# Kernel tuning notes

Measured on AMD Instinct MI355X. Metric: run time of the kernel, lower is better.

The kernel has to match this reference:

```python
import jax, jax.numpy as jnp
import numpy as np

B, L, W = 4096, 30, 5          # batch, MAX_TOKEN_LENGTH, WINDOW_SIZE
A, E = 30, 128                 # ALPHABET_SIZE, embedding dim
C = 40                         # OUT_CHANNELS
H, T = 128, 3                  # LSTM_UNITS, num CRF tags
LIN = W * C                    # 200
EPS = 1e-5


def setup_inputs():
    key = jax.random.key(0)
    ks = jax.random.split(key, 24)
    def rn(k, shape, s=0.1):
        return jax.random.normal(k, shape, jnp.float32) * s
    return {
        'x': jax.random.randint(ks[0], (B, L, W), 0, A, jnp.int32),
        'emb': rn(ks[1], (A, E), 1.0),
        'conv_w': rn(ks[2], (C, E, 3)),
        'conv_b': rn(ks[3], (C,)),
        'bn1_g': 1.0 + rn(ks[4], (C,)),
        'bn1_b': rn(ks[5], (C,)),
        'bn1_m': rn(ks[6], (C,)),
        'bn1_v': 0.5 + jax.random.uniform(ks[7], (C,), jnp.float32),
        'w_ih_f': rn(ks[8], (4 * H, LIN)),
        'w_hh_f': rn(ks[9], (4 * H, H)),
        'b_f': rn(ks[10], (4 * H,)),
        'w_ih_b': rn(ks[11], (4 * H, LIN)),
        'w_hh_b': rn(ks[12], (4 * H, H)),
        'b_b': rn(ks[13], (4 * H,)),
        'bn2_g': 1.0 + rn(ks[14], (2 * H,)),
        'bn2_b': rn(ks[15], (2 * H,)),
        'bn2_m': rn(ks[16], (2 * H,)),
        'bn2_v': 0.5 + jax.random.uniform(ks[17], (2 * H,), jnp.float32),
        'fc_w': rn(ks[18], (T, 2 * H)),
        'fc_b': rn(ks[19], (T,)),
        'trans': rn(ks[20], (T, T)),
        'start_t': rn(ks[21], (T,)),
        'end_t': rn(ks[22], (T,)),
    }


def _lstm_dir(seq, w_ih, w_hh, b, reverse):
    # seq: [B, L, F]; torch gate order i, f, g, o
    xs = jnp.einsum('blf,gf->lbg', seq, w_ih) + b  # [L, B, 4H]
    h0 = jnp.zeros((seq.shape[0], H), seq.dtype)
    def step(carry, xt):
        h, c = carry
        z = xt + h @ w_hh.T
        i, f, g, o = jnp.split(z, 4, axis=-1)
        c = jax.nn.sigmoid(f) * c + jax.nn.sigmoid(i) * jnp.tanh(g)
        h = jax.nn.sigmoid(o) * jnp.tanh(c)
        return (h, c), h
    _, hs = jax.lax.scan(step, (h0, h0), xs, reverse=reverse)
    return hs.transpose(1, 0, 2)  # [B, L, H]


def _viterbi(emis, mask, trans, start_t, end_t):
    # emis: [B, L, T], mask: [B, L] bool
    score = start_t + emis[:, 0]                      # [B, T]
    def step(score, inp):
        e_t, m_t = inp                                # [B, T], [B]
        cand = score[:, :, None] + trans              # [B, Tprev, Tnext]
        ptr = jnp.argmax(cand, axis=1)                # [B, T]
        new = jnp.max(cand, axis=1) + e_t
        return jnp.where(m_t[:, None], new, score), ptr
    score, hist = jax.lax.scan(
        step, score, (emis[:, 1:].transpose(1, 0, 2), mask[:, 1:].T))
    score = score + end_t
    best = jnp.max(score, axis=1)                     # [B] path scores
    last = jnp.argmax(score, axis=1)                  # [B]
    def back(tag, inp):
        h_t, m_t = inp
        prev = jnp.take_along_axis(h_t, tag[:, None], axis=1)[:, 0]
        tag = jnp.where(m_t, prev, tag)
        return tag, tag
    _, ys = jax.lax.scan(back, last, (hist, mask[:, 1:].T), reverse=True)
    tags = jnp.concatenate([ys, last[None]], axis=0).T  # [B, L]
    return best, tags


def reference(x, emb, conv_w, conv_b, bn1_g, bn1_b, bn1_m, bn1_v,
              w_ih_f, w_hh_f, b_f, w_ih_b, w_hh_b, b_b,
              bn2_g, bn2_b, bn2_m, bn2_v, fc_w, fc_b, trans, start_t, end_t):
    mask = x[:, :, 2] > 0                             # [B, L]
    e = emb[x.reshape(B * L, W)]                      # [N, W, E]  (dropout=eval noop)
    e = e.transpose(0, 2, 1)                          # [N, E, W]
    y = jax.lax.conv_general_dilated(
        e, conv_w, (1,), [(1, 1)],
        dimension_numbers=('NCH', 'OIH', 'NCH')) + conv_b[:, None]
    # BatchNorm1d (inference, running stats)
    y = (y - bn1_m[:, None]) * (bn1_g / jnp.sqrt(bn1_v + EPS))[:, None] + bn1_b[:, None]
    y = jax.nn.relu(y)
    # MaxPool1d(k=3, stride=1, pad=1): length preserved
    y = jax.lax.reduce_window(y, -jnp.inf, jax.lax.max,
                              (1, 1, 3), (1, 1, 1),
                              [(0, 0), (0, 0), (1, 1)])
    y = y.reshape(B, L, LIN)                          # torch.flatten is channel-major = row-major reshape
    hf = _lstm_dir(y, w_ih_f, w_hh_f, b_f, False)
    hb = _lstm_dir(y, w_ih_b, w_hh_b, b_b, True)
    h = jnp.concatenate([hf, hb], axis=-1)            # [B, L, 2H]
    h = (h - bn2_m) * (bn2_g / jnp.sqrt(bn2_v + EPS)) + bn2_b
    emis = h @ fc_w.T + fc_b                          # [B, L, T]
    return _viterbi(emis, mask, trans, start_t, end_t)
```

## Files before the change

kernel.cpp:

```cpp
#include <hip/hip_runtime.h>
#include <math.h>

#define BB    4096
#define LL    30
#define WW    5
#define CC    40
#define HH    128
#define TT    3
#define KA    328
#define NB    32
#define NT_   1024
#define FSTR  232
#define HSTR  136
#define CW    1056

#define WS_P    0
#define WS_BC   3600
#define WS_BG   3648
#define WS_WFC  4672
#define WS_EB   5440
#define WS_WBF  5504
#define WS_EMIS (5504 + 540672)

typedef __bf16 bf16x8 __attribute__((ext_vector_type(8)));
typedef float  f32x4  __attribute__((ext_vector_type(4)));
typedef unsigned short u16x8 __attribute__((ext_vector_type(8)));

__device__ __forceinline__ float sigm(float x) {
    return __builtin_amdgcn_rcpf(1.0f + __expf(-x));
}
__device__ __forceinline__ float tanh_fast(float x) {
    return 2.0f * __builtin_amdgcn_rcpf(1.0f + __expf(-2.0f * x)) - 1.0f;
}
__device__ __forceinline__ unsigned short f2bf(float f) {
    unsigned u = __builtin_bit_cast(unsigned, f);
    return (unsigned short)((u + 0x7FFFu + ((u >> 16) & 1u)) >> 16);
}
__device__ __forceinline__ float bf2f(unsigned short h) {
    unsigned u = ((unsigned)h) << 16;
    return __builtin_bit_cast(float, u);
}

__global__ void prep_kernel(const float* __restrict__ emb, const float* __restrict__ conv_w,
                            const float* __restrict__ conv_b,
                            const float* __restrict__ bn1_g, const float* __restrict__ bn1_b,
                            const float* __restrict__ bn1_m, const float* __restrict__ bn1_v,
                            const float* __restrict__ w_ih_f, const float* __restrict__ w_hh_f,
                            const float* __restrict__ b_f,
                            const float* __restrict__ w_ih_b, const float* __restrict__ w_hh_b,
                            const float* __restrict__ b_b,
                            const float* __restrict__ bn2_g, const float* __restrict__ bn2_b,
                            const float* __restrict__ bn2_m, const float* __restrict__ bn2_v,
                            const float* __restrict__ fc_w, const float* __restrict__ fc_b,
                            float* __restrict__ ws)
{
    const int gid = blockIdx.x * blockDim.x + threadIdx.x;
    const int gsz = gridDim.x * blockDim.x;

    for (int idx = gid; idx < 3600; idx += gsz) {
        int k = idx / 1200, rem = idx % 1200, a = rem / 40, c = rem % 40;
        float s1 = bn1_g[c] / sqrtf(bn1_v[c] + 1e-5f);
        float acc = 0.f;
        for (int e = 0; e < 128; ++e)
            acc += emb[a * 128 + e] * conv_w[(c * 128 + e) * 3 + k];
        ws[WS_P + idx] = acc * s1;
    }
    for (int c = gid; c < CC; c += gsz) {
        float s1 = bn1_g[c] / sqrtf(bn1_v[c] + 1e-5f);
        ws[WS_BC + c] = (conv_b[c] - bn1_m[c]) * s1 + bn1_b[c];
    }
    for (int i = gid; i < 1024; i += gsz) {
        int d = i >> 9, g = i & 511;
        ws[WS_BG + i] = d ? b_b[g] : b_f[g];
    }
    for (int i = gid; i < 768; i += gsz) {
        int d = i / 384, r = i % 384, t = r / 128, u = r % 128;
        int j = d * 128 + u;
        float s2 = bn2_g[j] / sqrtf(bn2_v[j] + 1e-5f);
        ws[WS_WFC + i] = fc_w[t * 256 + j] * s2;
    }
    for (int t = gid; t < TT; t += gsz) {
        float acc = fc_b[t];
        for (int j = 0; j < 256; ++j) {
            float s2 = bn2_g[j] / sqrtf(bn2_v[j] + 1e-5f);
            acc += fc_w[t * 256 + j] * (bn2_b[j] - bn2_m[j] * s2);
        }
        ws[WS_EB + t] = acc;
    }
    unsigned short* wsu = (unsigned short*)ws;
    for (int i = gid; i < 2 * 512 * CW; i += gsz) {
        int d = i / (512 * CW), r = i % (512 * CW);
        int n = r / CW, q = r % CW;
        int Ks = q / 96, t = q % 96, s = t / 32, k32 = t % 32;
        int k = Ks * 32 + k32;
        int u = n >> 2, g = n & 3, row = g * 128 + u;
        const float* wih = d ? w_ih_b : w_ih_f;
        const float* whh = d ? w_hh_b : w_hh_f;
        float w = (k < 200) ? wih[row * 200 + k]
                            : ((k >= 224) ? whh[row * 128 + (k - 224)] : 0.f);
        unsigned short t0 = f2bf(w);
        float r1 = w - bf2f(t0);
        unsigned short t1 = f2bf(r1);
        unsigned short t2 = f2bf(r1 - bf2f(t1));
        wsu[2 * WS_WBF + i] = (s == 0) ? t0 : ((s == 1) ? t1 : t2);
    }
}

__global__ __launch_bounds__(1024, 4)
void lstm_kernel(const int* __restrict__ x, float* __restrict__ ws)
{
    __shared__ unsigned short Fh[2][NB * FSTR], Fl[2][NB * FSTR], Fm[2][NB * FSTR];
    __shared__ unsigned short Hh[2][NB * HSTR], Hl[2][NB * HSTR], Hm[2][NB * HSTR];
    __shared__ float Pp_s[3600];
    __shared__ float Wfc_s[384];
    __shared__ float biasC_s[40];

    const int tid = threadIdx.x;
    const int d   = blockIdx.x & 1;
    const int b0  = (blockIdx.x >> 1) * NB;

    const unsigned short* __restrict__ Wb =
        (const unsigned short*)ws + 2 * WS_WBF + d * (512 * CW);
    float* emis = ws + WS_EMIS + d * (BB * LL * TT);

    for (int i = tid; i < 3600; i += NT_) Pp_s[i] = ws[WS_P + i];
    for (int i = tid; i < 384;  i += NT_) Wfc_s[i] = ws[WS_WFC + d * 384 + i];
    for (int i = tid; i < 40;   i += NT_) biasC_s[i] = ws[WS_BC + i];
    for (int i = tid; i < NB * FSTR; i += NT_) {
        ((unsigned*)Fh)[i] = 0u; ((unsigned*)Fl)[i] = 0u; ((unsigned*)Fm)[i] = 0u;
    }
    for (int i = tid; i < NB * HSTR; i += NT_) {
        ((unsigned*)Hh)[i] = 0u; ((unsigned*)Hl)[i] = 0u; ((unsigned*)Hm)[i] = 0u;
    }

    const int lane = tid & 63;
    const int wv   = tid >> 6;
    const int quad = lane >> 4;
    const int ml   = lane & 15;

    const unsigned short* __restrict__ Wn[2] = {
        Wb + (wv * 32 +  0 + ml) * CW + quad * 8,
        Wb + (wv * 32 + 16 + ml) * CW + quad * 8
    };

    const float* bgp = ws + WS_BG + d * 512;
    int   un[2];
    float bIv[2], bFv[2], bGv[2], bOv[2];
    #pragma unroll
    for (int nt = 0; nt < 2; ++nt) {
        int u = wv * 8 + nt * 4 + quad;
        un[nt]  = u;
        bIv[nt] = bgp[u];
        bFv[nt] = bgp[128 + u];
        bGv[nt] = bgp[256 + u];
        bOv[nt] = bgp[384 + u];
    }

    float cst[2][2];
    #pragma unroll
    for (int mt = 0; mt < 2; ++mt)
        #pragma unroll
        for (int nt = 0; nt < 2; ++nt) cst[mt][nt] = 0.f;

    __syncthreads();

#define FEAT_ONE(LPOS, BUF, P)                                                 \
    {                                                                          \
        int bb = (P) / CC, c = (P) % CC;                                       \
        const int* tok = x + (((b0 + bb) * LL) + (LPOS)) * WW;                 \
        int t0 = tok[0], t1 = tok[1], t2 = tok[2], t3 = tok[3], t4 = tok[4];   \
        float bc = biasC_s[c];                                                 \
        float a0 = bc + Pp_s[(30 + t0) * 40 + c] + Pp_s[(60 + t1) * 40 + c];   \
        float a1 = bc + Pp_s[t0 * 40 + c] + Pp_s[(30 + t1) * 40 + c] + Pp_s[(60 + t2) * 40 + c]; \
        float a2 = bc + Pp_s[t1 * 40 + c] + Pp_s[(30 + t2) * 40 + c] + Pp_s[(60 + t3) * 40 + c]; \
        float a3 = bc + Pp_s[t2 * 40 + c] + Pp_s[(30 + t3) * 40 + c] + Pp_s[(60 + t4) * 40 + c]; \
        float a4 = bc + Pp_s[t3 * 40 + c] + Pp_s[(30 + t4) * 40 + c];          \
        a0 = fmaxf(a0, 0.f); a1 = fmaxf(a1, 0.f); a2 = fmaxf(a2, 0.f);         \
        a3 = fmaxf(a3, 0.f); a4 = fmaxf(a4, 0.f);                              \
        float f[5];                                                            \
        f[0] = fmaxf(a0, a1);                                                  \
        f[1] = fmaxf(fmaxf(a0, a1), a2);                                       \
        f[2] = fmaxf(fmaxf(a1, a2), a3);                                       \
        f[3] = fmaxf(fmaxf(a2, a3), a4);                                       \
        f[4] = fmaxf(a3, a4);                                                  \
        int base = bb * FSTR + c * 5;                                          \
        _Pragma("unroll")                                                      \
        for (int j = 0; j < 5; ++j) {                                          \
            unsigned short h0 = f2bf(f[j]);                                    \
            float r1 = f[j] - bf2f(h0);                                        \
            unsigned short h1 = f2bf(r1);                                      \
            unsigned short h2 = f2bf(r1 - bf2f(h1));                           \
            Fh[BUF][base + j] = h0;                                            \
            Fl[BUF][base + j] = h1;                                            \
            Fm[BUF][base + j] = h2;                                            \
        }                                                                      \
    }

#define FEAT_BOTH(LPOS, BUF)                                                   \
    {                                                                          \
        FEAT_ONE(LPOS, BUF, tid)                                               \
        if (tid >= 768) FEAT_ONE(LPOS, BUF, tid + 256)                         \
    }

#define EMIS_BODY(LPOS, HB)                                                    \
    {                                                                          \
        int bb = tid / 6, r6 = tid % 6, t = r6 >> 1, seg = r6 & 1;             \
        int hoff = bb * HSTR + seg * 64;                                       \
        const float* wfc = &Wfc_s[t * 128 + seg * 64];                         \
        float s = 0.f;                                                         \
        _Pragma("unroll")                                                      \
        for (int i = 0; i < 8; ++i) {                                          \
            u16x8 v0 = *(const u16x8*)&Hh[HB][hoff + i * 8];                   \
            u16x8 v1 = *(const u16x8*)&Hl[HB][hoff + i * 8];                   \
            u16x8 v2 = *(const u16x8*)&Hm[HB][hoff + i * 8];                   \
            _Pragma("unroll")                                                  \
            for (int j = 0; j < 8; ++j) {                                      \
                float h = bf2f(v0[j]) + bf2f(v1[j]) + bf2f(v2[j]);             \
                s += h * wfc[i * 8 + j];                                       \
            }                                                                  \
        }                                                                      \
        s += __shfl_xor(s, 1);                                                 \
        if (seg == 0)                                                          \
            emis[(((b0 + bb) * LL) + (LPOS)) * TT + t] = s;                    \
    }

    {
        const int l0 = d ? (LL - 1) : 0;
        FEAT_BOTH(l0, 0)
    }
    __syncthreads();

    for (int step = 0; step < LL; ++step) {
        const int fb = step & 1;
        const int hw = step & 1;
        const int hr = hw ^ 1;

        f32x4 acc[2][2];
        #pragma unroll
        for (int mt = 0; mt < 2; ++mt)
            #pragma unroll
            for (int nt = 0; nt < 2; ++nt)
                acc[mt][nt] = (f32x4){0.f, 0.f, 0.f, 0.f};

#define WLOAD(B, P, KS)                                                        \
        {                                                                      \
            B[0] = *(const bf16x8*)((P) + (KS) * 96);                          \
            B[1] = *(const bf16x8*)((P) + (KS) * 96 + 32);                     \
            B[2] = *(const bf16x8*)((P) + (KS) * 96 + 64);                     \
        }
#define GEMM6(B, NT)                                                           \
        {                                                                      \
            acc[0][NT] = __builtin_amdgcn_mfma_f32_16x16x32_bf16(B[0], a0[0], acc[0][NT], 0, 0, 0); \
            acc[0][NT] = __builtin_amdgcn_mfma_f32_16x16x32_bf16(B[0], a0[1], acc[0][NT], 0, 0, 0); \
            acc[0][NT] = __builtin_amdgcn_mfma_f32_16x16x32_bf16(B[1], a0[0], acc[0][NT], 0, 0, 0); \
            acc[0][NT] = __builtin_amdgcn_mfma_f32_16x16x32_bf16(B[1], a0[1], acc[0][NT], 0, 0, 0); \
            acc[0][NT] = __builtin_amdgcn_mfma_f32_16x16x32_bf16(B[2], a0[0], acc[0][NT], 0, 0, 0); \
            acc[0][NT] = __builtin_amdgcn_mfma_f32_16x16x32_bf16(B[0], a0[2], acc[0][NT], 0, 0, 0); \
            acc[1][NT] = __builtin_amdgcn_mfma_f32_16x16x32_bf16(B[0], a1[0], acc[1][NT], 0, 0, 0); \
            acc[1][NT] = __builtin_amdgcn_mfma_f32_16x16x32_bf16(B[0], a1[1], acc[1][NT], 0, 0, 0); \
            acc[1][NT] = __builtin_amdgcn_mfma_f32_16x16x32_bf16(B[1], a1[0], acc[1][NT], 0, 0, 0); \
            acc[1][NT] = __builtin_amdgcn_mfma_f32_16x16x32_bf16(B[1], a1[1], acc[1][NT], 0, 0, 0); \
            acc[1][NT] = __builtin_amdgcn_mfma_f32_16x16x32_bf16(B[2], a1[0], acc[1][NT], 0, 0, 0); \
            acc[1][NT] = __builtin_amdgcn_mfma_f32_16x16x32_bf16(B[0], a1[2], acc[1][NT], 0, 0, 0); \
        }

        {
            bf16x8 wbuf[2][2][3];
            #pragma unroll
            for (int nt = 0; nt < 2; ++nt)
                WLOAD(wbuf[0][nt], Wn[nt], 0)

            #pragma unroll
            for (int Ks = 0; Ks < 11; ++Ks) {
                const int cur = Ks & 1, nxt = cur ^ 1;
                if (Ks < 10) {
                    #pragma unroll
                    for (int nt = 0; nt < 2; ++nt)
                        WLOAD(wbuf[nxt][nt], Wn[nt], Ks + 1)
                }
                bf16x8 a0[3], a1[3];
                if (Ks < 7) {
                    const int ko = Ks * 32 + quad * 8;
                    a0[0] = *(const bf16x8*)&Fh[fb][ml * FSTR + ko];
                    a0[1] = *(const bf16x8*)&Fl[fb][ml * FSTR + ko];
                    a0[2] = *(const bf16x8*)&Fm[fb][ml * FSTR + ko];
                    a1[0] = *(const bf16x8*)&Fh[fb][(16 + ml) * FSTR + ko];
                    a1[1] = *(const bf16x8*)&Fl[fb][(16 + ml) * FSTR + ko];
                    a1[2] = *(const bf16x8*)&Fm[fb][(16 + ml) * FSTR + ko];
                } else {
                    const int ko = (Ks - 7) * 32 + quad * 8;
                    a0[0] = *(const bf16x8*)&Hh[hr][ml * HSTR + ko];
                    a0[1] = *(const bf16x8*)&Hl[hr][ml * HSTR + ko];
                    a0[2] = *(const bf16x8*)&Hm[hr][ml * HSTR + ko];
                    a1[0] = *(const bf16x8*)&Hh[hr][(16 + ml) * HSTR + ko];
                    a1[1] = *(const bf16x8*)&Hl[hr][(16 + ml) * HSTR + ko];
                    a1[2] = *(const bf16x8*)&Hm[hr][(16 + ml) * HSTR + ko];
                }
                GEMM6(wbuf[cur][0], 0)
                GEMM6(wbuf[cur][1], 1)

                if (Ks == 4 && step + 1 < LL && (wv & 1) == 0) {
                    const int lnext = d ? (LL - 2 - step) : (step + 1);
                    FEAT_BOTH(lnext, fb ^ 1)
                }
                if (Ks == 8 && step + 1 < LL && (wv & 1) == 1) {
                    const int lnext = d ? (LL - 2 - step) : (step + 1);
                    FEAT_BOTH(lnext, fb ^ 1)
                }
            }
        }
#undef WLOAD
#undef GEMM6

        if (step > 0 && tid < 192) {
            const int lprev = d ? (LL - step) : (step - 1);
            EMIS_BODY(lprev, hr)
        }

        #pragma unroll
        for (int mt = 0; mt < 2; ++mt) {
            #pragma unroll
            for (int nt = 0; nt < 2; ++nt) {
                float zi = acc[mt][nt][0] + bIv[nt];
                float zf = acc[mt][nt][1] + bFv[nt];
                float zg = acc[mt][nt][2] + bGv[nt];
                float zo = acc[mt][nt][3] + bOv[nt];
                float cn = sigm(zf) * cst[mt][nt] + sigm(zi) * tanh_fast(zg);
                cst[mt][nt] = cn;
                float h = sigm(zo) * tanh_fast(cn);
                unsigned short h0 = f2bf(h);
                float r1 = h - bf2f(h0);
                unsigned short h1 = f2bf(r1);
                unsigned short h2 = f2bf(r1 - bf2f(h1));
                int idx = (mt * 16 + ml) * HSTR + un[nt];
                Hh[hw][idx] = h0;
                Hl[hw][idx] = h1;
                Hm[hw][idx] = h2;
            }
        }

        __syncthreads();
    }

    if (tid < 192) {
        const int llast = d ? 0 : (LL - 1);
        const int hl_ = (LL - 1) & 1;
        EMIS_BODY(llast, hl_)
    }
#undef EMIS_BODY
#undef FEAT_BOTH
#undef FEAT_ONE
}

__global__ void viterbi_kernel(const int* __restrict__ x, const float* __restrict__ ws,
                               const float* __restrict__ trans,
                               const float* __restrict__ start_t,
                               const float* __restrict__ end_t,
                               float* __restrict__ out)
{
    int b = blockIdx.x * blockDim.x + threadIdx.x;
    if (b >= BB) return;
    const float* eF = ws + WS_EMIS;
    const float* eB = ws + WS_EMIS + BB * LL * TT;
    const float eb0 = ws[WS_EB + 0], eb1 = ws[WS_EB + 1], eb2 = ws[WS_EB + 2];
    float tr[9];
    #pragma unroll
    for (int i = 0; i < 9; ++i) tr[i] = trans[i];

    int base = b * LL * TT;
    float s0 = start_t[0] + eF[base + 0] + eB[base + 0] + eb0;
    float s1 = start_t[1] + eF[base + 1] + eB[base + 1] + eb1;
    float s2 = start_t[2] + eF[base + 2] + eB[base + 2] + eb2;

    unsigned hist[LL - 1];
    unsigned maskbits = 0;

    #pragma unroll
    for (int l = 1; l < LL; ++l) {
        bool m = x[(b * LL + l) * WW + 2] > 0;
        if (m) maskbits |= (1u << l);
        int idx = base + l * TT;
        float e0 = eF[idx + 0] + eB[idx + 0] + eb0;
        float e1 = eF[idx + 1] + eB[idx + 1] + eb1;
        float e2 = eF[idx + 2] + eB[idx + 2] + eb2;

        float ns[3]; int pt[3];
        #pragma unroll
        for (int nt = 0; nt < 3; ++nt) {
            float c0 = s0 + tr[0 * 3 + nt];
            float c1 = s1 + tr[1 * 3 + nt];
            float c2 = s2 + tr[2 * 3 + nt];
            int p = 0; float bc = c0;
            if (c1 > bc) { bc = c1; p = 1; }
            if (c2 > bc) { bc = c2; p = 2; }
            ns[nt] = bc; pt[nt] = p;
        }
        ns[0] += e0; ns[1] += e1; ns[2] += e2;
        hist[l - 1] = (unsigned)pt[0] | ((unsigned)pt[1] << 2) | ((unsigned)pt[2] << 4);
        if (m) { s0 = ns[0]; s1 = ns[1]; s2 = ns[2]; }
    }
    s0 += end_t[0]; s1 += end_t[1]; s2 += end_t[2];
    float best = s0; int last = 0;
    if (s1 > best) { best = s1; last = 1; }
    if (s2 > best) { best = s2; last = 2; }

    out[b] = best;
    float* tags = out + BB + b * LL;
    int tag = last;
    tags[LL - 1] = (float)last;
    #pragma unroll
    for (int l = LL - 1; l >= 1; --l) {
        int prev = (int)((hist[l - 1] >> (2 * tag)) & 3u);
        if (maskbits & (1u << l)) tag = prev;
        tags[l - 1] = (float)tag;
    }
}

extern "C" void kernel_launch(void* const* d_in, const int* in_sizes, int n_in,
                              void* d_out, int out_size, void* d_ws, size_t ws_size,
                              hipStream_t stream)
{
    const int*   x      = (const int*)  d_in[0];
    const float* emb    = (const float*)d_in[1];
    const float* conv_w = (const float*)d_in[2];
    const float* conv_b = (const float*)d_in[3];
    const float* bn1_g  = (const float*)d_in[4];
    const float* bn1_b  = (const float*)d_in[5];
    const float* bn1_m  = (const float*)d_in[6];
    const float* bn1_v  = (const float*)d_in[7];
    const float* w_ih_f = (const float*)d_in[8];
    const float* w_hh_f = (const float*)d_in[9];
    const float* b_f    = (const float*)d_in[10];
    const float* w_ih_b = (const float*)d_in[11];
    const float* w_hh_b = (const float*)d_in[12];
    const float* b_b    = (const float*)d_in[13];
    const float* bn2_g  = (const float*)d_in[14];
    const float* bn2_b  = (const float*)d_in[15];
    const float* bn2_m  = (const float*)d_in[16];
    const float* bn2_v  = (const float*)d_in[17];
    const float* fc_w   = (const float*)d_in[18];
    const float* fc_b   = (const float*)d_in[19];
    const float* trans  = (const float*)d_in[20];
    const float* start_t= (const float*)d_in[21];
    const float* end_t  = (const float*)d_in[22];

    float* ws  = (float*)d_ws;
    float* out = (float*)d_out;

    prep_kernel<<<256, 256, 0, stream>>>(emb, conv_w, conv_b,
                                         bn1_g, bn1_b, bn1_m, bn1_v,
                                         w_ih_f, w_hh_f, b_f,
                                         w_ih_b, w_hh_b, b_b,
                                         bn2_g, bn2_b, bn2_m, bn2_v,
                                         fc_w, fc_b, ws);
    lstm_kernel<<<256, 1024, 0, stream>>>(x, ws);
    viterbi_kernel<<<16, 256, 0, stream>>>(x, ws, trans, start_t, end_t, out);
}
```

Baseline: 724.8 us.

## Software-pipeline LSTM steps: compute next step's input projection after recurrence

Restructures the recurrent loop so each step first does only the hidden-state GEMM (K-slices 7-10), runs the gate nonlinearities, then computes the next step's input-feature GEMM (K-slices 0-6) into a second accumulator set before the barrier. The loop is unrolled by two with ping-pong accumulators, and feature generation moves two steps ahead. The aim is to take the input-projection GEMM off the serial dependency chain between barriers and overlap it with the h writes. It costs more accumulator registers and a more complex buffer-index schedule.

Result: slower. 951.6 us (+31.3%).

```diff
diff --git a/kernel.cpp b/kernel.cpp
--- a/kernel.cpp
+++ b/kernel.cpp
@@ -224,129 +224,162 @@
             emis[(((b0 + bb) * LL) + (LPOS)) * TT + t] = s;                    \
     }
 
-    {
-        const int l0 = d ? (LL - 1) : 0;
-        FEAT_BOTH(l0, 0)
-    }
-    __syncthreads();
-
-    for (int step = 0; step < LL; ++step) {
-        const int fb = step & 1;
-        const int hw = step & 1;
-        const int hr = hw ^ 1;
-
-        f32x4 acc[2][2];
-        #pragma unroll
-        for (int mt = 0; mt < 2; ++mt)
-            #pragma unroll
-            for (int nt = 0; nt < 2; ++nt)
-                acc[mt][nt] = (f32x4){0.f, 0.f, 0.f, 0.f};
-
 #define WLOAD(B, P, KS)                                                        \
         {                                                                      \
             B[0] = *(const bf16x8*)((P) + (KS) * 96);                          \
             B[1] = *(const bf16x8*)((P) + (KS) * 96 + 32);                     \
             B[2] = *(const bf16x8*)((P) + (KS) * 96 + 64);                     \
         }
-#define GEMM6(B, NT)                                                           \
+#define GEMM6(B, ACC, NT)                                                      \
         {                                                                      \
-            acc[0][NT] = __builtin_amdgcn_mfma_f32_16x16x32_bf16(B[0], a0[0], acc[0][NT], 0, 0, 0); \
-            acc[0][NT] = __builtin_amdgcn_mfma_f32_16x16x32_bf16(B[0], a0[1], acc[0][NT], 0, 0, 0); \
-            acc[0][NT] = __builtin_amdgcn_mfma_f32_16x16x32_bf16(B[1], a0[0], acc[0][NT], 0, 0, 0); \
-            acc[0][NT] = __builtin_amdgcn_mfma_f32_16x16x32_bf16(B[1], a0[1], acc[0][NT], 0, 0, 0); \
-            acc[0][NT] = __builtin_amdgcn_mfma_f32_16x16x32_bf16(B[2], a0[0], acc[0][NT], 0, 0, 0); \
-            acc[0][NT] = __builtin_amdgcn_mfma_f32_16x16x32_bf16(B[0], a0[2], acc[0][NT], 0, 0, 0); \
-            acc[1][NT] = __builtin_amdgcn_mfma_f32_16x16x32_bf16(B[0], a1[0], acc[1][NT], 0, 0, 0); \
-            acc[1][NT] = __builtin_amdgcn_mfma_f32_16x16x32_bf16(B[0], a1[1], acc[1][NT], 0, 0, 0); \
-            acc[1][NT] = __builtin_amdgcn_mfma_f32_16x16x32_bf16(B[1], a1[0], acc[1][NT], 0, 0, 0); \
-            acc[1][NT] = __builtin_amdgcn_mfma_f32_16x16x32_bf16(B[1], a1[1], acc[1][NT], 0, 0, 0); \
-            acc[1][NT] = __builtin_amdgcn_mfma_f32_16x16x32_bf16(B[2], a1[0], acc[1][NT], 0, 0, 0); \
-            acc[1][NT] = __builtin_amdgcn_mfma_f32_16x16x32_bf16(B[0], a1[2], acc[1][NT], 0, 0, 0); \
+            ACC[0][NT] = __builtin_amdgcn_mfma_f32_16x16x32_bf16(B[0], a0[0], ACC[0][NT], 0, 0, 0); \
+            ACC[0][NT] = __builtin_amdgcn_mfma_f32_16x16x32_bf16(B[0], a0[1], ACC[0][NT], 0, 0, 0); \
+            ACC[0][NT] = __builtin_amdgcn_mfma_f32_16x16x32_bf16(B[1], a0[0], ACC[0][NT], 0, 0, 0); \
+            ACC[0][NT] = __builtin_amdgcn_mfma_f32_16x16x32_bf16(B[1], a0[1], ACC[0][NT], 0, 0, 0); \
+            ACC[0][NT] = __builtin_amdgcn_mfma_f32_16x16x32_bf16(B[2], a0[0], ACC[0][NT], 0, 0, 0); \
+            ACC[0][NT] = __builtin_amdgcn_mfma_f32_16x16x32_bf16(B[0], a0[2], ACC[0][NT], 0, 0, 0); \
+            ACC[1][NT] = __builtin_amdgcn_mfma_f32_16x16x32_bf16(B[0], a1[0], ACC[1][NT], 0, 0, 0); \
+            ACC[1][NT] = __builtin_amdgcn_mfma_f32_16x16x32_bf16(B[0], a1[1], ACC[1][NT], 0, 0, 0); \
+            ACC[1][NT] = __builtin_amdgcn_mfma_f32_16x16x32_bf16(B[1], a1[0], ACC[1][NT], 0, 0, 0); \
+            ACC[1][NT] = __builtin_amdgcn_mfma_f32_16x16x32_bf16(B[1], a1[1], ACC[1][NT], 0, 0, 0); \
+            ACC[1][NT] = __builtin_amdgcn_mfma_f32_16x16x32_bf16(B[2], a1[0], ACC[1][NT], 0, 0, 0); \
+            ACC[1][NT] = __builtin_amdgcn_mfma_f32_16x16x32_bf16(B[0], a1[2], ACC[1][NT], 0, 0, 0); \
         }
 
-        {
-            bf16x8 wbuf[2][2][3];
-            #pragma unroll
-            for (int nt = 0; nt < 2; ++nt)
-                WLOAD(wbuf[0][nt], Wn[nt], 0)
-
-            #pragma unroll
-            for (int Ks = 0; Ks < 11; ++Ks) {
-                const int cur = Ks & 1, nxt = cur ^ 1;
-                if (Ks < 10) {
-                    #pragma unroll
-                    for (int nt = 0; nt < 2; ++nt)
-                        WLOAD(wbuf[nxt][nt], Wn[nt], Ks + 1)
-                }
-                bf16x8 a0[3], a1[3];
-                if (Ks < 7) {
-                    const int ko = Ks * 32 + quad * 8;
-                    a0[0] = *(const bf16x8*)&Fh[fb][ml * FSTR + ko];
-                    a0[1] = *(const bf16x8*)&Fl[fb][ml * FSTR + ko];
-                    a0[2] = *(const bf16x8*)&Fm[fb][ml * FSTR + ko];
-                    a1[0] = *(const bf16x8*)&Fh[fb][(16 + ml) * FSTR + ko];
-                    a1[1] = *(const bf16x8*)&Fl[fb][(16 + ml) * FSTR + ko];
-                    a1[2] = *(const bf16x8*)&Fm[fb][(16 + ml) * FSTR + ko];
-                } else {
-                    const int ko = (Ks - 7) * 32 + quad * 8;
-                    a0[0] = *(const bf16x8*)&Hh[hr][ml * HSTR + ko];
-                    a0[1] = *(const bf16x8*)&Hl[hr][ml * HSTR + ko];
-                    a0[2] = *(const bf16x8*)&Hm[hr][ml * HSTR + ko];
-                    a1[0] = *(const bf16x8*)&Hh[hr][(16 + ml) * HSTR + ko];
-                    a1[1] = *(const bf16x8*)&Hl[hr][(16 + ml) * HSTR + ko];
-                    a1[2] = *(const bf16x8*)&Hm[hr][(16 + ml) * HSTR + ko];
-                }
-                GEMM6(wbuf[cur][0], 0)
-                GEMM6(wbuf[cur][1], 1)
-
-                if (Ks == 4 && step + 1 < LL && (wv & 1) == 0) {
-                    const int lnext = d ? (LL - 2 - step) : (step + 1);
-                    FEAT_BOTH(lnext, fb ^ 1)
-                }
-                if (Ks == 8 && step + 1 < LL && (wv & 1) == 1) {
-                    const int lnext = d ? (LL - 2 - step) : (step + 1);
-                    FEAT_BOTH(lnext, fb ^ 1)
-                }
-            }
-        }
-#undef WLOAD
-#undef GEMM6
-
-        if (step > 0 && tid < 192) {
-            const int lprev = d ? (LL - step) : (step - 1);
-            EMIS_BODY(lprev, hr)
-        }
-
+#define STEP_BODY(TT_, CUR, NXT, PB)                                           \
+    {                                                                          \
+        const int T_ = (TT_);                                                  \
+        const int hw = T_ & 1, hr = hw ^ 1;                                    \
+        _Pragma("unroll")                                                      \
+        for (int Ks = 7; Ks <= 10; ++Ks) {                                     \
+            const int cw_ = ((PB) + Ks - 7) & 1, nw_ = cw_ ^ 1;                \
+            const int lks = (Ks < 10) ? Ks + 1 : 0;                            \
+            _Pragma("unroll")                                                  \
+            for (int nt = 0; nt < 2; ++nt) WLOAD(wbuf[nw_][nt], Wn[nt], lks)   \
+            bf16x8 a0[3], a1[3];                                               \
+            const int ko = (Ks - 7) * 32 + quad * 8;                           \
+            a0[0] = *(const bf16x8*)&Hh[hr][ml * HSTR + ko];                   \
+            a0[1] = *(const bf16x8*)&Hl[hr][ml * HSTR + ko];                   \
+            a0[2] = *(const bf16x8*)&Hm[hr][ml * HSTR + ko];                   \
+            a1[0] = *(const bf16x8*)&Hh[hr][(16 + ml) * HSTR + ko];            \
+            a1[1] = *(const bf16x8*)&Hl[hr][(16 + ml) * HSTR + ko];            \
+            a1[2] = *(const bf16x8*)&Hm[hr][(16 + ml) * HSTR + ko];            \
+            GEMM6(wbuf[cw_][0], CUR, 0)                                        \
+            GEMM6(wbuf[cw_][1], CUR, 1)                                        \
+        }                                                                      \
+                  \
+        if (T_ > 0 && tid < 192) {                                             \
+            const int lprev = d ? (LL - T_) : (T_ - 1);                        \
+            EMIS_BODY(lprev, hr)                                               \
+        }                                                                      \
+            \
+        _Pragma("unroll")                                                      \
+        for (int mt = 0; mt < 2; ++mt) {                                       \
+            _Pragma("unroll")                                                  \
+            for (int nt = 0; nt < 2; ++nt) {                                   \
+                float zi = CUR[mt][nt][0] + bIv[nt];                           \
+                float zf = CUR[mt][nt][1] + bFv[nt];                           \
+                float zg = CUR[mt][nt][2] + bGv[nt];                           \
+                float zo = CUR[mt][nt][3] + bOv[nt];                           \
+                float cn = sigm(zf) * cst[mt][nt] + sigm(zi) * tanh_fast(zg);  \
+                cst[mt][nt] = cn;                                              \
+                float h = sigm(zo) * tanh_fast(cn);                            \
+                unsigned short h0 = f2bf(h);                                   \
+                float r1 = h - bf2f(h0);                                       \
+                unsigned short h1 = f2bf(r1);                                  \
+                unsigned short h2 = f2bf(r1 - bf2f(h1));                       \
+                int idx = (mt * 16 + ml) * HSTR + un[nt];                      \
+                Hh[hw][idx] = h0; Hl[hw][idx] = h1; Hm[hw][idx] = h2;          \
+            }                                                                  \
+        }                                                                      \
+          \
+        if (T_ + 1 < LL) {                                                     \
+            _Pragma("unroll")                                                  \
+            for (int mt = 0; mt < 2; ++mt)                                     \
+                _Pragma("unroll")                                              \
+                for (int nt = 0; nt < 2; ++nt)                                 \
+                    NXT[mt][nt] = (f32x4){0.f, 0.f, 0.f, 0.f};                 \
+            _Pragma("unroll")                                                  \
+            for (int Ks = 0; Ks <= 6; ++Ks) {                                  \
+                const int cw_ = ((PB) + Ks) & 1, nw_ = cw_ ^ 1;                \
+                _Pragma("unroll")                                              \
+                for (int nt = 0; nt < 2; ++nt) WLOAD(wbuf[nw_][nt], Wn[nt], Ks + 1) \
+                bf16x8 a0[3], a1[3];                                           \
+                const int ko = Ks * 32 + quad * 8;                             \
+                a0[0] = *(const bf16x8*)&Fh[hr][ml * FSTR + ko];               \
+                a0[1] = *(const bf16x8*)&Fl[hr][ml * FSTR + ko];               \
+                a0[2] = *(const bf16x8*)&Fm[hr][ml * FSTR + ko];               \
+                a1[0] = *(const bf16x8*)&Fh[hr][(16 + ml) * FSTR + ko];        \
+                a1[1] = *(const bf16x8*)&Fl[hr][(16 + ml) * FSTR + ko];        \
+                a1[2] = *(const bf16x8*)&Fm[hr][(16 + ml) * FSTR + ko];        \
+                GEMM6(wbuf[cw_][0], NXT, 0)                                    \
+                GEMM6(wbuf[cw_][1], NXT, 1)                                    \
+                 \
+                if (Ks == 1 && T_ + 2 < LL && (wv & 1) == 0) {                 \
+                    const int ln2 = d ? (LL - 3 - T_) : (T_ + 2);              \
+                    FEAT_BOTH(ln2, hw)                                         \
+                }                                                              \
+                if (Ks == 4 && T_ + 2 < LL && (wv & 1) == 1) {                 \
+                    const int ln2 = d ? (LL - 3 - T_) : (T_ + 2);              \
+                    FEAT_BOTH(ln2, hw)                                         \
+                }                                                              \
+            }                                                                  \
+        }                                                                      \
+        __syncthreads();                                                       \
+    }
+
+    {
+        const int l0 = d ? (LL - 1) : 0;
+        FEAT_BOTH(l0, 0)
+    }
+    __syncthreads();
+
+    f32x4 accA[2][2], accB[2][2];
+    #pragma unroll
+    for (int mt = 0; mt < 2; ++mt)
         #pragma unroll
-        for (int mt = 0; mt < 2; ++mt) {
-            #pragma unroll
-            for (int nt = 0; nt < 2; ++nt) {
-                float zi = acc[mt][nt][0] + bIv[nt];
-                float zf = acc[mt][nt][1] + bFv[nt];
-                float zg = acc[mt][nt][2] + bGv[nt];
-                float zo = acc[mt][nt][3] + bOv[nt];
-                float cn = sigm(zf) * cst[mt][nt] + sigm(zi) * tanh_fast(zg);
-                cst[mt][nt] = cn;
-                float h = sigm(zo) * tanh_fast(cn);
-                unsigned short h0 = f2bf(h);
-                float r1 = h - bf2f(h0);
-                unsigned short h1 = f2bf(r1);
-                unsigned short h2 = f2bf(r1 - bf2f(h1));
-                int idx = (mt * 16 + ml) * HSTR + un[nt];
-                Hh[hw][idx] = h0;
-                Hl[hw][idx] = h1;
-                Hm[hw][idx] = h2;
-            }
-        }
-
-        __syncthreads();
+        for (int nt = 0; nt < 2; ++nt)
+            accA[mt][nt] = (f32x4){0.f, 0.f, 0.f, 0.f};
+
+    bf16x8 wbuf[2][2][3];
+    #pragma unroll
+    for (int nt = 0; nt < 2; ++nt)
+        WLOAD(wbuf[0][nt], Wn[nt], 0)
+
+    #pragma unroll
+    for (int Ks = 0; Ks <= 6; ++Ks) {
+        const int cw_ = Ks & 1, nw_ = cw_ ^ 1;
+        #pragma unroll
+        for (int nt = 0; nt < 2; ++nt) WLOAD(wbuf[nw_][nt], Wn[nt], Ks + 1)
+        bf16x8 a0[3], a1[3];
+        const int ko = Ks * 32 + quad * 8;
+        a0[0] = *(const bf16x8*)&Fh[0][ml * FSTR + ko];
+        a0[1] = *(const bf16x8*)&Fl[0][ml * FSTR + ko];
+        a0[2] = *(const bf16x8*)&Fm[0][ml * FSTR + ko];
+        a1[0] = *(const bf16x8*)&Fh[0][(16 + ml) * FSTR + ko];
+        a1[1] = *(const bf16x8*)&Fl[0][(16 + ml) * FSTR + ko];
+        a1[2] = *(const bf16x8*)&Fm[0][(16 + ml) * FSTR + ko];
+        GEMM6(wbuf[cw_][0], accA, 0)
+        GEMM6(wbuf[cw_][1], accA, 1)
+    }
+    {
+        const int l1 = d ? (LL - 2) : 1;
+        FEAT_BOTH(l1, 1)
+    }
+    __syncthreads();
+
+    for (int t2 = 0; t2 < LL / 2; ++t2) {
+        STEP_BODY(2 * t2,     accA, accB, 1)
+        STEP_BODY(2 * t2 + 1, accB, accA, 0)
     }
 
     if (tid < 192) {
         const int llast = d ? 0 : (LL - 1);
-        const int hl_ = (LL - 1) & 1;
-        EMIS_BODY(llast, hl_)
-    }
+        EMIS_BODY(llast, 1)
+    }
+#undef STEP_BODY
+#undef GEMM6
+#undef WLOAD
 #undef EMIS_BODY
 #undef FEAT_BOTH
 #undef FEAT_ONE
```
